# Optimization experiments

Hardware: AMD Instinct MI355X
Metric: run time of the kernel (lower is better)

## Reference

```python
import jax, jax.numpy as jnp
import numpy as np

K_VALUES = (2, 4, 8)  # sorted k_values from init


def setup_inputs() -> dict:
    key = jax.random.key(0)
    ks = jax.random.split(key, 6)
    B, T, D, H = 16, 2048, 512, 64
    nk = len(K_VALUES)
    # columns: (E, Pt, eta, phi) -- E,Pt positive, eta in [-3,3], phi in [-pi,pi]
    u = jax.random.uniform(ks[0], (B, T, 4), jnp.float32)
    tokens_cont = u * jnp.array([100.0, 50.0, 6.0, 6.2832], jnp.float32) + jnp.array([1.0, 1.0, -3.0, -3.1416], jnp.float32)
    lengths = jax.random.randint(ks[1], (B,), T // 2, T + 1)
    mask = jnp.arange(T)[None, :] < lengths[:, None]  # [B,T] True=valid
    W1 = jax.random.normal(ks[2], (nk, H), jnp.float32) / np.sqrt(nk).astype(np.float32)
    b1 = jax.random.normal(ks[3], (H,), jnp.float32) * 0.01
    W2 = jax.random.normal(ks[4], (H, D), jnp.float32) / np.sqrt(H).astype(np.float32)
    b2 = jax.random.normal(ks[5], (D,), jnp.float32) * 0.01
    return dict(tokens_cont=tokens_cont, mask=mask, W1=W1, b1=b1, W2=W2, b2=b2)


def reference(tokens_cont, mask, W1, b1, W2, b2):
    B, T, _ = tokens_cont.shape
    E, Pt, eta, phi = (tokens_cont[..., i] for i in range(4))
    px = Pt * jnp.cos(phi)
    py = Pt * jnp.sin(phi)
    pz = Pt * jnp.sinh(jnp.clip(eta, -20.0, 20.0))
    P = jnp.stack([E, px, py, pz], axis=-1)  # [B,T,4] four-momentum
    metric = jnp.array([1.0, -1.0, -1.0, -1.0], P.dtype)
    # Lorentz dot: E_i E_j - px_i px_j - py_i py_j - pz_i pz_j -> [B,T,T]
    dot = jnp.einsum('btc,bsc->bts', P * metric, P)
    dot = jnp.where(mask[:, None, :], dot, -jnp.inf)  # exclude padding friends
    max_k = min(max(K_VALUES), T)
    _, topk_idx = jax.lax.top_k(dot, max_k)  # [B,T,max_k]
    Pf = P[jnp.arange(B)[:, None, None], topk_idx]  # gather friends [B,T,max_k,4]
    cum = jnp.cumsum(Pf, axis=2)  # prefix sums over sorted friends
    masses = []
    maskf = mask.astype(P.dtype)
    for k in K_VALUES:
        ps = cum[:, :, min(k, max_k) - 1, :]  # [B,T,4] summed 4-momentum of top-k group
        m2 = ps[..., 0] ** 2 - jnp.sum(ps[..., 1:] ** 2, axis=-1)
        m2 = jnp.maximum(m2, 0.0) * maskf
        masses.append(jnp.sqrt(m2 + 1e-8))
    mass = jnp.stack(masses, axis=-1)  # [B,T,n_k]
    h = jax.nn.gelu(mass @ W1 + b1, approximate=False)  # torch GELU = exact erf
    return h @ W2 + b2  # [B,T,model_dim]
```

## Files before the change

kernel.cpp:

```cpp
#include <hip/hip_runtime.h>
#include <hip/hip_bf16.h>
#include <math.h>

#define NB 16
#define NT 2048
#define ND 512
#define NH 64

typedef __attribute__((ext_vector_type(8))) short short8;
typedef __attribute__((ext_vector_type(4))) float float4v;

__device__ __forceinline__ bool mask_is_bytes(const int* m) {
    return m[0] == 0x01010101;
}
__device__ __forceinline__ bool mask_at(const int* m, bool bytes, int i) {
    if (bytes) return ((const unsigned char*)m)[i] != 0;
    return m[i] != 0;
}

__device__ __forceinline__ float dot4(float4 a, float4 p) {
    float d = a.x * p.x;
    d = __builtin_fmaf(a.y, p.y, d);
    d = __builtin_fmaf(a.z, p.z, d);
    d = __builtin_fmaf(a.w, p.w, d);
    return d;
}

__device__ __forceinline__ unsigned short f2bf(float x) {
    unsigned int u = __float_as_uint(x);
    u += 0x7fffu + ((u >> 16) & 1u);
    return (unsigned short)(u >> 16);
}

__global__ void __launch_bounds__(256) prep_kernel(
        const float* __restrict__ tok, const int* __restrict__ mask,
        const float* __restrict__ W2, unsigned short* __restrict__ W2t,
        float4* __restrict__ Pg) {
    int i = blockIdx.x * 256 + threadIdx.x;
    if (i < ND * NH) {
        int n = i & (ND - 1), k = i >> 9;
        W2t[n * NH + k] = f2bf(W2[k * ND + n]);
    } else {
        int j = i - ND * NH;
        const bool mb = mask_is_bytes(mask);
        float4 tv = ((const float4*)tok)[j];
        bool m = mask_at(mask, mb, j);
        float E = tv.x, Pt = tv.y, eta = tv.z, phi = tv.w;
        float px = Pt * cosf(phi);
        float py = Pt * sinf(phi);
        float pz = Pt * sinhf(fminf(fmaxf(eta, -20.f), 20.f));
        Pg[j] = m ? make_float4(E, px, py, pz)
                  : make_float4(-1e30f, 0.f, 0.f, 0.f);
    }
}

#define VT(w2, j, l)  scratch[((w2) * 8 + (j)) * 64 + (l)]
#define PS(w2, c, l)  scratch[((w2) * 12 + (c)) * 64 + (l)]

__global__ void __launch_bounds__(512) fused_topk_mass_mlp_kernel(
        const int* __restrict__ mask,
        const float* __restrict__ W1,
        const float* __restrict__ b1,
        const unsigned short* __restrict__ W2t,
        const float* __restrict__ b2,
        const float4* __restrict__ Pg,
        float* __restrict__ out) {
    __shared__ float scratch[8 * 12 * 64];
    __shared__ unsigned short hs[64][88];
    __shared__ float mass_s[3][64];
    __shared__ int wcnt[8];

    const int b    = blockIdx.y;
    const int t0   = blockIdx.x * 64;
    const int tid  = threadIdx.x;
    const int lane = tid & 63;
    const int w    = tid >> 6;
    const bool mb  = mask_is_bytes(mask);

    const bool blockValid = mask_at(mask, mb, b * NT + t0);

    if (blockValid) {
        int cnt = 0;
#pragma unroll
        for (int it = 0; it < 4; ++it) {
            int i = tid + it * 512;
            bool m = mask_at(mask, mb, b * NT + i);
            cnt += (int)__popcll(__ballot(m));
        }
        if (lane == 0) wcnt[w] = cnt;
        __syncthreads();

        int L = 0;
#pragma unroll
        for (int j = 0; j < 8; ++j) L += wcnt[j];
        const int C    = (L + 7) >> 3;
        const int sBeg = w * C;
        const int sEnd = min(sBeg + C, L);

        const float4* Pb = Pg + (size_t)b * NT;
        float4 pt = Pb[t0 + lane];
        float4 a  = make_float4(pt.x, -pt.y, -pt.z, -pt.w);

        const float NEGBIG = -3.402823466e38f;
        float v0 = NEGBIG, v1 = NEGBIG, v2 = NEGBIG, v3 = NEGBIG;
        float v4 = NEGBIG, v5 = NEGBIG, v6 = NEGBIG, v7 = NEGBIG;

#pragma unroll 8
        for (int s = sBeg; s < sEnd; ++s) {
            float4 ps = Pb[__builtin_amdgcn_readfirstlane(s)];
            float d = dot4(a, ps);
            float n0 = fmaxf(v0, d);
            float n1 = __builtin_amdgcn_fmed3f(d, v0, v1);
            float n2 = __builtin_amdgcn_fmed3f(d, v1, v2);
            float n3 = __builtin_amdgcn_fmed3f(d, v2, v3);
            float n4 = __builtin_amdgcn_fmed3f(d, v3, v4);
            float n5 = __builtin_amdgcn_fmed3f(d, v4, v5);
            float n6 = __builtin_amdgcn_fmed3f(d, v5, v6);
            float n7 = __builtin_amdgcn_fmed3f(d, v6, v7);
            v0 = n0; v1 = n1; v2 = n2; v3 = n3;
            v4 = n4; v5 = n5; v6 = n6; v7 = n7;
        }
        VT(w, 0, lane) = v0; VT(w, 1, lane) = v1;
        VT(w, 2, lane) = v2; VT(w, 3, lane) = v3;
        VT(w, 4, lane) = v4; VT(w, 5, lane) = v5;
        VT(w, 6, lane) = v6; VT(w, 7, lane) = v7;
        __syncthreads();

        float m0 = NEGBIG, m1 = NEGBIG, m2_ = NEGBIG, m3 = NEGBIG;
        float m4 = NEGBIG, m5 = NEGBIG, m6 = NEGBIG, m7 = NEGBIG;
#pragma unroll
        for (int w2 = 0; w2 < 8; ++w2) {
#pragma unroll
            for (int j = 0; j < 8; ++j) {
                float d = VT(w2, j, lane);
                float n0 = fmaxf(m0, d);
                float n1 = __builtin_amdgcn_fmed3f(d, m0, m1);
                float n2 = __builtin_amdgcn_fmed3f(d, m1, m2_);
                float n3 = __builtin_amdgcn_fmed3f(d, m2_, m3);
                float n4 = __builtin_amdgcn_fmed3f(d, m3, m4);
                float n5 = __builtin_amdgcn_fmed3f(d, m4, m5);
                float n6 = __builtin_amdgcn_fmed3f(d, m5, m6);
                float n7 = __builtin_amdgcn_fmed3f(d, m6, m7);
                m0 = n0; m1 = n1; m2_ = n2; m3 = n3;
                m4 = n4; m5 = n5; m6 = n6; m7 = n7;
            }
        }
        const float th2 = m1, th4 = m3, th8 = m7;
        __syncthreads();

        float s2x = 0.f, s2y = 0.f, s2z = 0.f, s2w = 0.f;
        float s4x = 0.f, s4y = 0.f, s4z = 0.f, s4w = 0.f;
        float s8x = 0.f, s8y = 0.f, s8z = 0.f, s8w = 0.f;
#pragma unroll 4
        for (int s = sBeg; s < sEnd; ++s) {
            float4 ps = Pb[__builtin_amdgcn_readfirstlane(s)];
            float d = dot4(a, ps);
            if (d >= th8) {
                s8x += ps.x; s8y += ps.y; s8z += ps.z; s8w += ps.w;
                if (d >= th4) {
                    s4x += ps.x; s4y += ps.y; s4z += ps.z; s4w += ps.w;
                    if (d >= th2) {
                        s2x += ps.x; s2y += ps.y; s2z += ps.z; s2w += ps.w;
                    }
                }
            }
        }
        PS(w, 0, lane) = s2x;  PS(w, 1, lane) = s2y;
        PS(w, 2, lane) = s2z;  PS(w, 3, lane) = s2w;
        PS(w, 4, lane) = s4x;  PS(w, 5, lane) = s4y;
        PS(w, 6, lane) = s4z;  PS(w, 7, lane) = s4w;
        PS(w, 8, lane) = s8x;  PS(w, 9, lane) = s8y;
        PS(w, 10, lane) = s8z; PS(w, 11, lane) = s8w;
        __syncthreads();

        if (w == 0) {
            float tot[12];
#pragma unroll
            for (int c = 0; c < 12; ++c) {
                float acc = 0.f;
#pragma unroll
                for (int w2 = 0; w2 < 8; ++w2) acc += PS(w2, c, lane);
                tot[c] = acc;
            }
            const bool maskt = (t0 + lane) < L;
            const float MZ = sqrtf(1e-8f);
            auto massf = [&](float sx, float sy, float sz, float sw) -> float {
                float q = sx * sx;
                q = __builtin_fmaf(-sy, sy, q);
                q = __builtin_fmaf(-sz, sz, q);
                q = __builtin_fmaf(-sw, sw, q);
                q = fmaxf(q, 0.f);
                return sqrtf(q + 1e-8f);
            };
            mass_s[0][lane] = maskt ? massf(tot[0], tot[1], tot[2], tot[3]) : MZ;
            mass_s[1][lane] = maskt ? massf(tot[4], tot[5], tot[6], tot[7]) : MZ;
            mass_s[2][lane] = maskt ? massf(tot[8], tot[9], tot[10], tot[11]) : MZ;
        }
    } else {
        if (tid < 64) {
            const float MZ = sqrtf(1e-8f);
            mass_s[0][tid] = MZ;
            mass_s[1][tid] = MZ;
            mass_s[2][tid] = MZ;
        }
    }
    __syncthreads();

    {
        const int tt = lane;
        const int hr = w;
        float q0 = mass_s[0][tt];
        float q1 = mass_s[1][tt];
        float q2 = mass_s[2][tt];
        unsigned short hv[8];
#pragma unroll
        for (int j = 0; j < 8; ++j) {
            int hh = hr * 8 + j;
            float pre = b1[hh];
            pre = __builtin_fmaf(q0, W1[hh], pre);
            pre = __builtin_fmaf(q1, W1[NH + hh], pre);
            pre = __builtin_fmaf(q2, W1[2 * NH + hh], pre);
            float g = 0.5f * pre * (1.0f + erff(pre * 0.70710678118654752f));
            hv[j] = f2bf(g);
        }
        *(short8*)&hs[tt][hr * 8] = *(const short8*)hv;
    }
    __syncthreads();

    const int col   = lane & 15;
    const int quad  = lane >> 4;
    const int mhalf = w >> 2;
    const int nBase = (w & 3) * 128;

    short8 afrag[2][2];
#pragma unroll
    for (int mt = 0; mt < 2; ++mt)
#pragma unroll
        for (int ks = 0; ks < 2; ++ks)
            afrag[mt][ks] = *(const short8*)&hs[mhalf * 32 + mt * 16 + col][ks * 32 + quad * 8];

    float4v acc[2][8];
#pragma unroll
    for (int mt = 0; mt < 2; ++mt)
#pragma unroll
        for (int nt = 0; nt < 8; ++nt)
            acc[mt][nt] = (float4v)(0.f);

#pragma unroll
    for (int nt = 0; nt < 8; ++nt) {
        const unsigned short* wp = W2t + (nBase + nt * 16 + col) * NH + quad * 8;
        short8 bf0 = *(const short8*)(wp);
        short8 bf1 = *(const short8*)(wp + 32);
        acc[0][nt] = __builtin_amdgcn_mfma_f32_16x16x32_bf16(afrag[0][0], bf0, acc[0][nt], 0, 0, 0);
        acc[1][nt] = __builtin_amdgcn_mfma_f32_16x16x32_bf16(afrag[1][0], bf0, acc[1][nt], 0, 0, 0);
        acc[0][nt] = __builtin_amdgcn_mfma_f32_16x16x32_bf16(afrag[0][1], bf1, acc[0][nt], 0, 0, 0);
        acc[1][nt] = __builtin_amdgcn_mfma_f32_16x16x32_bf16(afrag[1][1], bf1, acc[1][nt], 0, 0, 0);
    }

#pragma unroll
    for (int nt = 0; nt < 8; ++nt) {
        float bias = b2[nBase + nt * 16 + col];
#pragma unroll
        for (int mt = 0; mt < 2; ++mt) {
            int mRow = b * NT + t0 + mhalf * 32 + mt * 16 + quad * 4;
            size_t base = (size_t)mRow * ND + nBase + nt * 16 + col;
#pragma unroll
            for (int r = 0; r < 4; ++r) {
                out[base + (size_t)r * ND] = acc[mt][nt][r] + bias;
            }
        }
    }
}

extern "C" void kernel_launch(void* const* d_in, const int* in_sizes, int n_in,
                              void* d_out, int out_size, void* d_ws, size_t ws_size,
                              hipStream_t stream) {
    const float* tok  = (const float*)d_in[0];
    const int*   mask = (const int*)d_in[1];
    const float* W1   = (const float*)d_in[2];
    const float* b1   = (const float*)d_in[3];
    const float* W2   = (const float*)d_in[4];
    const float* b2   = (const float*)d_in[5];
    float*       out  = (float*)d_out;

    unsigned short* W2t = (unsigned short*)d_ws;
    float4*         Pg  = (float4*)((char*)d_ws + 0x10000);

    prep_kernel<<<dim3((ND * NH + NB * NT) / 256), dim3(256), 0, stream>>>(
        tok, mask, W2, W2t, Pg);

    dim3 gB(NT / 64, NB);
    fused_topk_mass_mlp_kernel<<<gB, dim3(512), 0, stream>>>(
        mask, W1, b1, W2t, b2, Pg, out);
}
```

Baseline: 163.6 us.

## Remap top-k search to one query per wave with register-cached candidates

Each wave now handles 8 queries one at a time. All 2048 candidate four-momenta are cached in registers, 32 per lane, and spread across the 64 lanes. The per-lane top-8 is merged by eight rounds of DPP wave-max pops, and the group sums are reduced with DPP wave sums, so the shared-memory scratch and the block-wide syncs for merging go away. The cost is much more serialized cross-lane work per query and heavy register pressure from the 32 float4 values per lane, which could hurt occupancy despite the launch_bounds(512,2) hint.

```diff
diff --git a/kernel.cpp b/kernel.cpp
--- a/kernel.cpp
+++ b/kernel.cpp
@@ -18,18 +18,37 @@
     return m[i] != 0;
 }
 
-__device__ __forceinline__ float dot4(float4 a, float4 p) {
-    float d = a.x * p.x;
-    d = __builtin_fmaf(a.y, p.y, d);
-    d = __builtin_fmaf(a.z, p.z, d);
-    d = __builtin_fmaf(a.w, p.w, d);
-    return d;
-}
-
 __device__ __forceinline__ unsigned short f2bf(float x) {
     unsigned int u = __float_as_uint(x);
     u += 0x7fffu + ((u >> 16) & 1u);
     return (unsigned short)(u >> 16);
+}
+
+__device__ __forceinline__ float rlane(float x, int j) {
+    return __int_as_float(__builtin_amdgcn_readlane(__float_as_int(x), j));
+}
+
+template <int CTRL>
+__device__ __forceinline__ float updpp(float x, int identBits) {
+    return __int_as_float(__builtin_amdgcn_update_dpp(
+        identBits, __float_as_int(x), CTRL, 0xF, 0xF, false));
+}
+__device__ __forceinline__ float wave_max(float m) {
+    const int NI = (int)0xFF800000u;
+    m = fmaxf(m, updpp<0x111>(m, NI));
+    m = fmaxf(m, updpp<0x112>(m, NI));
+    m = fmaxf(m, updpp<0x114>(m, NI));
+    m = fmaxf(m, updpp<0x118>(m, NI));
+    float a = rlane(m, 15), bb = rlane(m, 31);
+    float c = rlane(m, 47), d  = rlane(m, 63);
+    return fmaxf(fmaxf(a, bb), fmaxf(c, d));
+}
+__device__ __forceinline__ float wave_sum(float x) {
+    x += updpp<0x111>(x, 0);
+    x += updpp<0x112>(x, 0);
+    x += updpp<0x114>(x, 0);
+    x += updpp<0x118>(x, 0);
+    return (rlane(x, 15) + rlane(x, 31)) + (rlane(x, 47) + rlane(x, 63));
 }
 
 __global__ void __launch_bounds__(256) prep_kernel(
@@ -54,10 +73,7 @@
     }
 }
 
-#define VT(w2, j, l)  scratch[((w2) * 8 + (j)) * 64 + (l)]
-#define PS(w2, c, l)  scratch[((w2) * 12 + (c)) * 64 + (l)]
-
-__global__ void __launch_bounds__(512) fused_topk_mass_mlp_kernel(
+__global__ void __launch_bounds__(512, 2) fused_topk_mass_mlp_kernel(
         const int* __restrict__ mask,
         const float* __restrict__ W1,
         const float* __restrict__ b1,
@@ -65,7 +81,6 @@
         const float* __restrict__ b2,
         const float4* __restrict__ Pg,
         float* __restrict__ out) {
-    __shared__ float scratch[8 * 12 * 64];
     __shared__ unsigned short hs[64][88];
     __shared__ float mass_s[3][64];
     __shared__ int wcnt[8];
@@ -76,6 +91,8 @@
     const int lane = tid & 63;
     const int w    = tid >> 6;
     const bool mb  = mask_is_bytes(mask);
+    const float NEGBIG = -3.402823466e38f;
+    const float MZ = sqrtf(1e-8f);
 
     const bool blockValid = mask_at(mask, mb, b * NT + t0);
 
@@ -84,121 +101,128 @@
 #pragma unroll
         for (int it = 0; it < 4; ++it) {
             int i = tid + it * 512;
-            bool m = mask_at(mask, mb, b * NT + i);
-            cnt += (int)__popcll(__ballot(m));
+            cnt += (int)__popcll(__ballot(mask_at(mask, mb, b * NT + i)));
         }
         if (lane == 0) wcnt[w] = cnt;
         __syncthreads();
-
         int L = 0;
 #pragma unroll
         for (int j = 0; j < 8; ++j) L += wcnt[j];
-        const int C    = (L + 7) >> 3;
-        const int sBeg = w * C;
-        const int sEnd = min(sBeg + C, L);
-
-        const float4* Pb = Pg + (size_t)b * NT;
+        const int RACT = (L + 63) >> 6;
+
+        const float4* __restrict__ Pb = Pg + (size_t)b * NT;
         float4 pt = Pb[t0 + lane];
-        float4 a  = make_float4(pt.x, -pt.y, -pt.z, -pt.w);
-
-        const float NEGBIG = -3.402823466e38f;
-        float v0 = NEGBIG, v1 = NEGBIG, v2 = NEGBIG, v3 = NEGBIG;
-        float v4 = NEGBIG, v5 = NEGBIG, v6 = NEGBIG, v7 = NEGBIG;
-
-#pragma unroll 8
-        for (int s = sBeg; s < sEnd; ++s) {
-            float4 ps = Pb[__builtin_amdgcn_readfirstlane(s)];
-            float d = dot4(a, ps);
-            float n0 = fmaxf(v0, d);
-            float n1 = __builtin_amdgcn_fmed3f(d, v0, v1);
-            float n2 = __builtin_amdgcn_fmed3f(d, v1, v2);
-            float n3 = __builtin_amdgcn_fmed3f(d, v2, v3);
-            float n4 = __builtin_amdgcn_fmed3f(d, v3, v4);
-            float n5 = __builtin_amdgcn_fmed3f(d, v4, v5);
-            float n6 = __builtin_amdgcn_fmed3f(d, v5, v6);
-            float n7 = __builtin_amdgcn_fmed3f(d, v6, v7);
-            v0 = n0; v1 = n1; v2 = n2; v3 = n3;
-            v4 = n4; v5 = n5; v6 = n6; v7 = n7;
-        }
-        VT(w, 0, lane) = v0; VT(w, 1, lane) = v1;
-        VT(w, 2, lane) = v2; VT(w, 3, lane) = v3;
-        VT(w, 4, lane) = v4; VT(w, 5, lane) = v5;
-        VT(w, 6, lane) = v6; VT(w, 7, lane) = v7;
-        __syncthreads();
-
-        float m0 = NEGBIG, m1 = NEGBIG, m2_ = NEGBIG, m3 = NEGBIG;
-        float m4 = NEGBIG, m5 = NEGBIG, m6 = NEGBIG, m7 = NEGBIG;
-#pragma unroll
-        for (int w2 = 0; w2 < 8; ++w2) {
-#pragma unroll
-            for (int j = 0; j < 8; ++j) {
-                float d = VT(w2, j, lane);
-                float n0 = fmaxf(m0, d);
-                float n1 = __builtin_amdgcn_fmed3f(d, m0, m1);
-                float n2 = __builtin_amdgcn_fmed3f(d, m1, m2_);
-                float n3 = __builtin_amdgcn_fmed3f(d, m2_, m3);
-                float n4 = __builtin_amdgcn_fmed3f(d, m3, m4);
-                float n5 = __builtin_amdgcn_fmed3f(d, m4, m5);
-                float n6 = __builtin_amdgcn_fmed3f(d, m5, m6);
-                float n7 = __builtin_amdgcn_fmed3f(d, m6, m7);
-                m0 = n0; m1 = n1; m2_ = n2; m3 = n3;
-                m4 = n4; m5 = n5; m6 = n6; m7 = n7;
+
+        float4 cr[32];
+#pragma unroll
+        for (int r = 0; r < 32; ++r) cr[r] = Pb[r * 64 + lane];
+
+#pragma unroll 1
+        for (int q = 0; q < 8; ++q) {
+            const int ql = w * 8 + q;
+            if (t0 + ql < L) {
+                const float Eq  =  rlane(pt.x, ql);
+                const float npx = -rlane(pt.y, ql);
+                const float npy = -rlane(pt.z, ql);
+                const float npz = -rlane(pt.w, ql);
+
+                float v0 = NEGBIG, v1 = NEGBIG, v2 = NEGBIG, v3 = NEGBIG;
+                float v4 = NEGBIG, v5 = NEGBIG, v6 = NEGBIG, v7 = NEGBIG;
+#pragma unroll
+                for (int r = 0; r < 32; ++r) {
+                    if (r < RACT) {
+                        float d = Eq * cr[r].x;
+                        d = __builtin_fmaf(npx, cr[r].y, d);
+                        d = __builtin_fmaf(npy, cr[r].z, d);
+                        d = __builtin_fmaf(npz, cr[r].w, d);
+                        float n0 = fmaxf(v0, d);
+                        float n1 = __builtin_amdgcn_fmed3f(d, v0, v1);
+                        float n2 = __builtin_amdgcn_fmed3f(d, v1, v2);
+                        float n3 = __builtin_amdgcn_fmed3f(d, v2, v3);
+                        float n4 = __builtin_amdgcn_fmed3f(d, v3, v4);
+                        float n5 = __builtin_amdgcn_fmed3f(d, v4, v5);
+                        float n6 = __builtin_amdgcn_fmed3f(d, v5, v6);
+                        float n7 = __builtin_amdgcn_fmed3f(d, v6, v7);
+                        v0 = n0; v1 = n1; v2 = n2; v3 = n3;
+                        v4 = n4; v5 = n5; v6 = n6; v7 = n7;
+                    }
+                }
+
+                float th2 = NEGBIG, th4 = NEGBIG, th8 = NEGBIG;
+#pragma unroll
+                for (int round = 1; round <= 8; ++round) {
+                    float gm = wave_max(v0);
+                    if (round == 2) th2 = gm;
+                    if (round == 4) th4 = gm;
+                    if (round == 8) th8 = gm;
+                    if (round < 8) {
+                        bool pop = (v0 == gm);
+                        v0 = pop ? v1 : v0;
+                        v1 = pop ? v2 : v1;
+                        v2 = pop ? v3 : v2;
+                        v3 = pop ? v4 : v3;
+                        v4 = pop ? v5 : v4;
+                        v5 = pop ? v6 : v5;
+                        v6 = pop ? v7 : v6;
+                        v7 = pop ? NEGBIG : v7;
+                    }
+                }
+
+                float s2x = 0.f, s2y = 0.f, s2z = 0.f, s2w = 0.f;
+                float s4x = 0.f, s4y = 0.f, s4z = 0.f, s4w = 0.f;
+                float s8x = 0.f, s8y = 0.f, s8z = 0.f, s8w = 0.f;
+#pragma unroll
+                for (int r = 0; r < 32; ++r) {
+                    if (r < RACT) {
+                        float d = Eq * cr[r].x;
+                        d = __builtin_fmaf(npx, cr[r].y, d);
+                        d = __builtin_fmaf(npy, cr[r].z, d);
+                        d = __builtin_fmaf(npz, cr[r].w, d);
+                        if (d >= th8) {
+                            s8x += cr[r].x; s8y += cr[r].y;
+                            s8z += cr[r].z; s8w += cr[r].w;
+                            if (d >= th4) {
+                                s4x += cr[r].x; s4y += cr[r].y;
+                                s4z += cr[r].z; s4w += cr[r].w;
+                                if (d >= th2) {
+                                    s2x += cr[r].x; s2y += cr[r].y;
+                                    s2z += cr[r].z; s2w += cr[r].w;
+                                }
+                            }
+                        }
+                    }
+                }
+
+                float t2x = wave_sum(s2x), t2y = wave_sum(s2y);
+                float t2z = wave_sum(s2z), t2w = wave_sum(s2w);
+                float t4x = wave_sum(s4x), t4y = wave_sum(s4y);
+                float t4z = wave_sum(s4z), t4w = wave_sum(s4w);
+                float t8x = wave_sum(s8x), t8y = wave_sum(s8y);
+                float t8z = wave_sum(s8z), t8w = wave_sum(s8w);
+
+                auto massf = [&](float sx, float sy, float sz, float sw) -> float {
+                    float qq = sx * sx;
+                    qq = __builtin_fmaf(-sy, sy, qq);
+                    qq = __builtin_fmaf(-sz, sz, qq);
+                    qq = __builtin_fmaf(-sw, sw, qq);
+                    qq = fmaxf(qq, 0.f);
+                    return sqrtf(qq + 1e-8f);
+                };
+                if (lane == 0) {
+                    mass_s[0][ql] = massf(t2x, t2y, t2z, t2w);
+                    mass_s[1][ql] = massf(t4x, t4y, t4z, t4w);
+                    mass_s[2][ql] = massf(t8x, t8y, t8z, t8w);
+                }
+            } else {
+                if (lane == 0) {
+                    mass_s[0][ql] = MZ;
+                    mass_s[1][ql] = MZ;
+                    mass_s[2][ql] = MZ;
+                }
             }
-        }
-        const float th2 = m1, th4 = m3, th8 = m7;
-        __syncthreads();
-
-        float s2x = 0.f, s2y = 0.f, s2z = 0.f, s2w = 0.f;
-        float s4x = 0.f, s4y = 0.f, s4z = 0.f, s4w = 0.f;
-        float s8x = 0.f, s8y = 0.f, s8z = 0.f, s8w = 0.f;
-#pragma unroll 4
-        for (int s = sBeg; s < sEnd; ++s) {
-            float4 ps = Pb[__builtin_amdgcn_readfirstlane(s)];
-            float d = dot4(a, ps);
-            if (d >= th8) {
-                s8x += ps.x; s8y += ps.y; s8z += ps.z; s8w += ps.w;
-                if (d >= th4) {
-                    s4x += ps.x; s4y += ps.y; s4z += ps.z; s4w += ps.w;
-                    if (d >= th2) {
-                        s2x += ps.x; s2y += ps.y; s2z += ps.z; s2w += ps.w;
-                    }
-                }
-            }
-        }
-        PS(w, 0, lane) = s2x;  PS(w, 1, lane) = s2y;
-        PS(w, 2, lane) = s2z;  PS(w, 3, lane) = s2w;
-        PS(w, 4, lane) = s4x;  PS(w, 5, lane) = s4y;
-        PS(w, 6, lane) = s4z;  PS(w, 7, lane) = s4w;
-        PS(w, 8, lane) = s8x;  PS(w, 9, lane) = s8y;
-        PS(w, 10, lane) = s8z; PS(w, 11, lane) = s8w;
-        __syncthreads();
-
-        if (w == 0) {
-            float tot[12];
-#pragma unroll
-            for (int c = 0; c < 12; ++c) {
-                float acc = 0.f;
-#pragma unroll
-                for (int w2 = 0; w2 < 8; ++w2) acc += PS(w2, c, lane);
-                tot[c] = acc;
-            }
-            const bool maskt = (t0 + lane) < L;
-            const float MZ = sqrtf(1e-8f);
-            auto massf = [&](float sx, float sy, float sz, float sw) -> float {
-                float q = sx * sx;
-                q = __builtin_fmaf(-sy, sy, q);
-                q = __builtin_fmaf(-sz, sz, q);
-                q = __builtin_fmaf(-sw, sw, q);
-                q = fmaxf(q, 0.f);
-                return sqrtf(q + 1e-8f);
-            };
-            mass_s[0][lane] = maskt ? massf(tot[0], tot[1], tot[2], tot[3]) : MZ;
-            mass_s[1][lane] = maskt ? massf(tot[4], tot[5], tot[6], tot[7]) : MZ;
-            mass_s[2][lane] = maskt ? massf(tot[8], tot[9], tot[10], tot[11]) : MZ;
         }
     } else {
         if (tid < 64) {
-            const float MZ = sqrtf(1e-8f);
             mass_s[0][tid] = MZ;
             mass_s[1][tid] = MZ;
             mass_s[2][tid] = MZ;
```

Measured after the change: 184.9 us. 13.0% more time.

## Pair query tiles per block and stage batch four-momenta in LDS

Applied to the files above, without the earlier changes.

Each block now handles two 64-token query tiles, one from the first half and one from the second half of the sequence. Pairing them balances work across blocks, since every block gets an always-valid tile A plus a tile B that may be padding. The whole batch's four-momenta are copied into LDS once, and each candidate load is shared between both query tiles in the top-k and accumulation passes. The cost is a much larger LDS footprint (about 80KB), which lowers occupancy, plus more registers for the doubled chains and a serialized two-pass MLP epilogue.

```diff
diff --git a/kernel.cpp b/kernel.cpp
--- a/kernel.cpp
+++ b/kernel.cpp
@@ -31,6 +31,19 @@
     u += 0x7fffu + ((u >> 16) & 1u);
     return (unsigned short)(u >> 16);
 }
+
+#define CHAIN8(v0,v1,v2,v3,v4,v5,v6,v7,d) do {                 \
+    float n0 = fmaxf(v0, d);                                    \
+    float n1 = __builtin_amdgcn_fmed3f(d, v0, v1);              \
+    float n2 = __builtin_amdgcn_fmed3f(d, v1, v2);              \
+    float n3 = __builtin_amdgcn_fmed3f(d, v2, v3);              \
+    float n4 = __builtin_amdgcn_fmed3f(d, v3, v4);              \
+    float n5 = __builtin_amdgcn_fmed3f(d, v4, v5);              \
+    float n6 = __builtin_amdgcn_fmed3f(d, v5, v6);              \
+    float n7 = __builtin_amdgcn_fmed3f(d, v6, v7);              \
+    v0 = n0; v1 = n1; v2 = n2; v3 = n3;                         \
+    v4 = n4; v5 = n5; v6 = n6; v7 = n7;                         \
+} while (0)
 
 __global__ void __launch_bounds__(256) prep_kernel(
         const float* __restrict__ tok, const int* __restrict__ mask,
@@ -54,8 +67,10 @@
     }
 }
 
-#define VT(w2, j, l)  scratch[((w2) * 8 + (j)) * 64 + (l)]
-#define PS(w2, c, l)  scratch[((w2) * 12 + (c)) * 64 + (l)]
+#define VTA(w2, j, l)  scratch[((w2) * 8 + (j)) * 64 + (l)]
+#define VTB(w2, j, l)  scratch[4096 + ((w2) * 8 + (j)) * 64 + (l)]
+#define PSA(w2, c, l)  scratch[((w2) * 12 + (c)) * 64 + (l)]
+#define PSB(w2, c, l)  scratch[6144 + ((w2) * 12 + (c)) * 64 + (l)]
 
 __global__ void __launch_bounds__(512) fused_topk_mass_mlp_kernel(
         const int* __restrict__ mask,
@@ -65,165 +80,216 @@
         const float* __restrict__ b2,
         const float4* __restrict__ Pg,
         float* __restrict__ out) {
-    __shared__ float scratch[8 * 12 * 64];
-    __shared__ unsigned short hs[64][88];
-    __shared__ float mass_s[3][64];
+    __shared__ __align__(16) unsigned char smem_raw[32768 + 49152];
     __shared__ int wcnt[8];
+    float* Plds            = (float*)smem_raw;
+    float* scratch         = (float*)(smem_raw + 32768);
+    unsigned short (*hs)[88] = (unsigned short(*)[88])smem_raw;
+    float (*mass_s)[128]   = (float(*)[128])(smem_raw + 12288);
 
     const int b    = blockIdx.y;
-    const int t0   = blockIdx.x * 64;
+    const int x    = blockIdx.x;
+    const int tA   = 64 * x;
+    const int tB   = 1024 + 64 * x;
     const int tid  = threadIdx.x;
     const int lane = tid & 63;
     const int w    = tid >> 6;
     const bool mb  = mask_is_bytes(mask);
-
-    const bool blockValid = mask_at(mask, mb, b * NT + t0);
-
-    if (blockValid) {
-        int cnt = 0;
-#pragma unroll
-        for (int it = 0; it < 4; ++it) {
-            int i = tid + it * 512;
-            bool m = mask_at(mask, mb, b * NT + i);
-            cnt += (int)__popcll(__ballot(m));
-        }
-        if (lane == 0) wcnt[w] = cnt;
-        __syncthreads();
-
-        int L = 0;
-#pragma unroll
-        for (int j = 0; j < 8; ++j) L += wcnt[j];
-        const int C    = (L + 7) >> 3;
-        const int sBeg = w * C;
-        const int sEnd = min(sBeg + C, L);
-
-        const float4* Pb = Pg + (size_t)b * NT;
-        float4 pt = Pb[t0 + lane];
-        float4 a  = make_float4(pt.x, -pt.y, -pt.z, -pt.w);
-
-        const float NEGBIG = -3.402823466e38f;
-        float v0 = NEGBIG, v1 = NEGBIG, v2 = NEGBIG, v3 = NEGBIG;
-        float v4 = NEGBIG, v5 = NEGBIG, v6 = NEGBIG, v7 = NEGBIG;
-
-#pragma unroll 8
+    const float NEGBIG = -3.402823466e38f;
+    const float MZ = sqrtf(1e-8f);
+
+    int cnt = 0;
+    const float4* __restrict__ Pb = Pg + (size_t)b * NT;
+#pragma unroll
+    for (int it = 0; it < 4; ++it) {
+        int i = tid + it * 512;
+        *(float4*)&Plds[i * 4] = Pb[i];
+        cnt += (int)__popcll(__ballot(mask_at(mask, mb, b * NT + i)));
+    }
+    if (lane == 0) wcnt[w] = cnt;
+    __syncthreads();
+
+    int L = 0;
+#pragma unroll
+    for (int j = 0; j < 8; ++j) L += wcnt[j];
+    const int C    = (L + 7) >> 3;
+    const int sBeg = w * C;
+    const int sEnd = min(sBeg + C, L);
+    const bool hasB = tB < L;
+
+    float4 pA = *(const float4*)&Plds[(tA + lane) * 4];
+    float4 pBq = *(const float4*)&Plds[(tB + lane) * 4];
+    float4 aA = make_float4(pA.x, -pA.y, -pA.z, -pA.w);
+    float4 aB = make_float4(pBq.x, -pBq.y, -pBq.z, -pBq.w);
+
+    float vA0 = NEGBIG, vA1 = NEGBIG, vA2 = NEGBIG, vA3 = NEGBIG;
+    float vA4 = NEGBIG, vA5 = NEGBIG, vA6 = NEGBIG, vA7 = NEGBIG;
+    float vB0 = NEGBIG, vB1 = NEGBIG, vB2 = NEGBIG, vB3 = NEGBIG;
+    float vB4 = NEGBIG, vB5 = NEGBIG, vB6 = NEGBIG, vB7 = NEGBIG;
+
+    if (hasB) {
+#pragma unroll 4
         for (int s = sBeg; s < sEnd; ++s) {
-            float4 ps = Pb[__builtin_amdgcn_readfirstlane(s)];
-            float d = dot4(a, ps);
-            float n0 = fmaxf(v0, d);
-            float n1 = __builtin_amdgcn_fmed3f(d, v0, v1);
-            float n2 = __builtin_amdgcn_fmed3f(d, v1, v2);
-            float n3 = __builtin_amdgcn_fmed3f(d, v2, v3);
-            float n4 = __builtin_amdgcn_fmed3f(d, v3, v4);
-            float n5 = __builtin_amdgcn_fmed3f(d, v4, v5);
-            float n6 = __builtin_amdgcn_fmed3f(d, v5, v6);
-            float n7 = __builtin_amdgcn_fmed3f(d, v6, v7);
-            v0 = n0; v1 = n1; v2 = n2; v3 = n3;
-            v4 = n4; v5 = n5; v6 = n6; v7 = n7;
-        }
-        VT(w, 0, lane) = v0; VT(w, 1, lane) = v1;
-        VT(w, 2, lane) = v2; VT(w, 3, lane) = v3;
-        VT(w, 4, lane) = v4; VT(w, 5, lane) = v5;
-        VT(w, 6, lane) = v6; VT(w, 7, lane) = v7;
-        __syncthreads();
-
+            float4 ps = *(const float4*)&Plds[s * 4];
+            float dA = dot4(aA, ps);
+            float dB = dot4(aB, ps);
+            CHAIN8(vA0, vA1, vA2, vA3, vA4, vA5, vA6, vA7, dA);
+            CHAIN8(vB0, vB1, vB2, vB3, vB4, vB5, vB6, vB7, dB);
+        }
+    } else {
+#pragma unroll 4
+        for (int s = sBeg; s < sEnd; ++s) {
+            float4 ps = *(const float4*)&Plds[s * 4];
+            float dA = dot4(aA, ps);
+            CHAIN8(vA0, vA1, vA2, vA3, vA4, vA5, vA6, vA7, dA);
+        }
+    }
+    VTA(w, 0, lane) = vA0; VTA(w, 1, lane) = vA1;
+    VTA(w, 2, lane) = vA2; VTA(w, 3, lane) = vA3;
+    VTA(w, 4, lane) = vA4; VTA(w, 5, lane) = vA5;
+    VTA(w, 6, lane) = vA6; VTA(w, 7, lane) = vA7;
+    if (hasB) {
+        VTB(w, 0, lane) = vB0; VTB(w, 1, lane) = vB1;
+        VTB(w, 2, lane) = vB2; VTB(w, 3, lane) = vB3;
+        VTB(w, 4, lane) = vB4; VTB(w, 5, lane) = vB5;
+        VTB(w, 6, lane) = vB6; VTB(w, 7, lane) = vB7;
+    }
+    __syncthreads();
+
+    float thA2, thA4, thA8;
+    {
         float m0 = NEGBIG, m1 = NEGBIG, m2_ = NEGBIG, m3 = NEGBIG;
         float m4 = NEGBIG, m5 = NEGBIG, m6 = NEGBIG, m7 = NEGBIG;
 #pragma unroll
-        for (int w2 = 0; w2 < 8; ++w2) {
+        for (int w2 = 0; w2 < 8; ++w2)
 #pragma unroll
             for (int j = 0; j < 8; ++j) {
-                float d = VT(w2, j, lane);
-                float n0 = fmaxf(m0, d);
-                float n1 = __builtin_amdgcn_fmed3f(d, m0, m1);
-                float n2 = __builtin_amdgcn_fmed3f(d, m1, m2_);
-                float n3 = __builtin_amdgcn_fmed3f(d, m2_, m3);
-                float n4 = __builtin_amdgcn_fmed3f(d, m3, m4);
-                float n5 = __builtin_amdgcn_fmed3f(d, m4, m5);
-                float n6 = __builtin_amdgcn_fmed3f(d, m5, m6);
-                float n7 = __builtin_amdgcn_fmed3f(d, m6, m7);
-                m0 = n0; m1 = n1; m2_ = n2; m3 = n3;
-                m4 = n4; m5 = n5; m6 = n6; m7 = n7;
-            }
-        }
-        const float th2 = m1, th4 = m3, th8 = m7;
-        __syncthreads();
-
-        float s2x = 0.f, s2y = 0.f, s2z = 0.f, s2w = 0.f;
-        float s4x = 0.f, s4y = 0.f, s4z = 0.f, s4w = 0.f;
-        float s8x = 0.f, s8y = 0.f, s8z = 0.f, s8w = 0.f;
+                float d = VTA(w2, j, lane);
+                CHAIN8(m0, m1, m2_, m3, m4, m5, m6, m7, d);
+            }
+        thA2 = m1; thA4 = m3; thA8 = m7;
+    }
+    float thB2 = 0.f, thB4 = 0.f, thB8 = 0.f;
+    if (hasB) {
+        float m0 = NEGBIG, m1 = NEGBIG, m2_ = NEGBIG, m3 = NEGBIG;
+        float m4 = NEGBIG, m5 = NEGBIG, m6 = NEGBIG, m7 = NEGBIG;
+#pragma unroll
+        for (int w2 = 0; w2 < 8; ++w2)
+#pragma unroll
+            for (int j = 0; j < 8; ++j) {
+                float d = VTB(w2, j, lane);
+                CHAIN8(m0, m1, m2_, m3, m4, m5, m6, m7, d);
+            }
+        thB2 = m1; thB4 = m3; thB8 = m7;
+    }
+    __syncthreads();
+
+    {
+        float a2x = 0.f, a2y = 0.f, a2z = 0.f, a2w = 0.f;
+        float a4x = 0.f, a4y = 0.f, a4z = 0.f, a4w = 0.f;
+        float a8x = 0.f, a8y = 0.f, a8z = 0.f, a8w = 0.f;
+        float b2x = 0.f, b2y = 0.f, b2z = 0.f, b2w = 0.f;
+        float b4x = 0.f, b4y = 0.f, b4z = 0.f, b4w = 0.f;
+        float b8x = 0.f, b8y = 0.f, b8z = 0.f, b8w = 0.f;
+        if (hasB) {
 #pragma unroll 4
-        for (int s = sBeg; s < sEnd; ++s) {
-            float4 ps = Pb[__builtin_amdgcn_readfirstlane(s)];
-            float d = dot4(a, ps);
-            if (d >= th8) {
-                s8x += ps.x; s8y += ps.y; s8z += ps.z; s8w += ps.w;
-                if (d >= th4) {
-                    s4x += ps.x; s4y += ps.y; s4z += ps.z; s4w += ps.w;
-                    if (d >= th2) {
-                        s2x += ps.x; s2y += ps.y; s2z += ps.z; s2w += ps.w;
+            for (int s = sBeg; s < sEnd; ++s) {
+                float4 ps = *(const float4*)&Plds[s * 4];
+                float dA = dot4(aA, ps);
+                float dB = dot4(aB, ps);
+                if (dA >= thA8) {
+                    a8x += ps.x; a8y += ps.y; a8z += ps.z; a8w += ps.w;
+                    if (dA >= thA4) {
+                        a4x += ps.x; a4y += ps.y; a4z += ps.z; a4w += ps.w;
+                        if (dA >= thA2) {
+                            a2x += ps.x; a2y += ps.y; a2z += ps.z; a2w += ps.w;
+                        }
                     }
                 }
-            }
-        }
-        PS(w, 0, lane) = s2x;  PS(w, 1, lane) = s2y;
-        PS(w, 2, lane) = s2z;  PS(w, 3, lane) = s2w;
-        PS(w, 4, lane) = s4x;  PS(w, 5, lane) = s4y;
-        PS(w, 6, lane) = s4z;  PS(w, 7, lane) = s4w;
-        PS(w, 8, lane) = s8x;  PS(w, 9, lane) = s8y;
-        PS(w, 10, lane) = s8z; PS(w, 11, lane) = s8w;
-        __syncthreads();
-
+                if (dB >= thB8) {
+                    b8x += ps.x; b8y += ps.y; b8z += ps.z; b8w += ps.w;
+                    if (dB >= thB4) {
+                        b4x += ps.x; b4y += ps.y; b4z += ps.z; b4w += ps.w;
+                        if (dB >= thB2) {
+                            b2x += ps.x; b2y += ps.y; b2z += ps.z; b2w += ps.w;
+                        }
+                    }
+                }
+            }
+        } else {
+#pragma unroll 4
+            for (int s = sBeg; s < sEnd; ++s) {
+                float4 ps = *(const float4*)&Plds[s * 4];
+                float dA = dot4(aA, ps);
+                if (dA >= thA8) {
+                    a8x += ps.x; a8y += ps.y; a8z += ps.z; a8w += ps.w;
+                    if (dA >= thA4) {
+                        a4x += ps.x; a4y += ps.y; a4z += ps.z; a4w += ps.w;
+                        if (dA >= thA2) {
+                            a2x += ps.x; a2y += ps.y; a2z += ps.z; a2w += ps.w;
+                        }
+                    }
+                }
+            }
+        }
+        PSA(w, 0, lane) = a2x;  PSA(w, 1, lane) = a2y;
+        PSA(w, 2, lane) = a2z;  PSA(w, 3, lane) = a2w;
+        PSA(w, 4, lane) = a4x;  PSA(w, 5, lane) = a4y;
+        PSA(w, 6, lane) = a4z;  PSA(w, 7, lane) = a4w;
+        PSA(w, 8, lane) = a8x;  PSA(w, 9, lane) = a8y;
+        PSA(w, 10, lane) = a8z; PSA(w, 11, lane) = a8w;
+        if (hasB) {
+            PSB(w, 0, lane) = b2x;  PSB(w, 1, lane) = b2y;
+            PSB(w, 2, lane) = b2z;  PSB(w, 3, lane) = b2w;
+            PSB(w, 4, lane) = b4x;  PSB(w, 5, lane) = b4y;
+            PSB(w, 6, lane) = b4z;  PSB(w, 7, lane) = b4w;
+            PSB(w, 8, lane) = b8x;  PSB(w, 9, lane) = b8y;
+            PSB(w, 10, lane) = b8z; PSB(w, 11, lane) = b8w;
+        }
+    }
+    __syncthreads();
+
+    {
+        auto massf = [](float sx, float sy, float sz, float sw) -> float {
+            float q = sx * sx;
+            q = __builtin_fmaf(-sy, sy, q);
+            q = __builtin_fmaf(-sz, sz, q);
+            q = __builtin_fmaf(-sw, sw, q);
+            q = fmaxf(q, 0.f);
+            return sqrtf(q + 1e-8f);
+        };
         if (w == 0) {
             float tot[12];
 #pragma unroll
             for (int c = 0; c < 12; ++c) {
                 float acc = 0.f;
 #pragma unroll
-                for (int w2 = 0; w2 < 8; ++w2) acc += PS(w2, c, lane);
+                for (int w2 = 0; w2 < 8; ++w2) acc += PSA(w2, c, lane);
                 tot[c] = acc;
             }
-            const bool maskt = (t0 + lane) < L;
-            const float MZ = sqrtf(1e-8f);
-            auto massf = [&](float sx, float sy, float sz, float sw) -> float {
-                float q = sx * sx;
-                q = __builtin_fmaf(-sy, sy, q);
-                q = __builtin_fmaf(-sz, sz, q);
-                q = __builtin_fmaf(-sw, sw, q);
-                q = fmaxf(q, 0.f);
-                return sqrtf(q + 1e-8f);
-            };
-            mass_s[0][lane] = maskt ? massf(tot[0], tot[1], tot[2], tot[3]) : MZ;
-            mass_s[1][lane] = maskt ? massf(tot[4], tot[5], tot[6], tot[7]) : MZ;
-            mass_s[2][lane] = maskt ? massf(tot[8], tot[9], tot[10], tot[11]) : MZ;
-        }
-    } else {
-        if (tid < 64) {
-            const float MZ = sqrtf(1e-8f);
-            mass_s[0][tid] = MZ;
-            mass_s[1][tid] = MZ;
-            mass_s[2][tid] = MZ;
-        }
-    }
-    __syncthreads();
-
-    {
-        const int tt = lane;
-        const int hr = w;
-        float q0 = mass_s[0][tt];
-        float q1 = mass_s[1][tt];
-        float q2 = mass_s[2][tt];
-        unsigned short hv[8];
-#pragma unroll
-        for (int j = 0; j < 8; ++j) {
-            int hh = hr * 8 + j;
-            float pre = b1[hh];
-            pre = __builtin_fmaf(q0, W1[hh], pre);
-            pre = __builtin_fmaf(q1, W1[NH + hh], pre);
-            pre = __builtin_fmaf(q2, W1[2 * NH + hh], pre);
-            float g = 0.5f * pre * (1.0f + erff(pre * 0.70710678118654752f));
-            hv[j] = f2bf(g);
-        }
-        *(short8*)&hs[tt][hr * 8] = *(const short8*)hv;
+            mass_s[0][lane] = massf(tot[0], tot[1], tot[2], tot[3]);
+            mass_s[1][lane] = massf(tot[4], tot[5], tot[6], tot[7]);
+            mass_s[2][lane] = massf(tot[8], tot[9], tot[10], tot[11]);
+        } else if (w == 1) {
+            if (hasB) {
+                float tot[12];
+#pragma unroll
+                for (int c = 0; c < 12; ++c) {
+                    float acc = 0.f;
+#pragma unroll
+                    for (int w2 = 0; w2 < 8; ++w2) acc += PSB(w2, c, lane);
+                    tot[c] = acc;
+                }
+                const bool maskt = (tB + lane) < L;
+                mass_s[0][64 + lane] = maskt ? massf(tot[0], tot[1], tot[2], tot[3]) : MZ;
+                mass_s[1][64 + lane] = maskt ? massf(tot[4], tot[5], tot[6], tot[7]) : MZ;
+                mass_s[2][64 + lane] = maskt ? massf(tot[8], tot[9], tot[10], tot[11]) : MZ;
+            } else {
+                mass_s[0][64 + lane] = MZ;
+                mass_s[1][64 + lane] = MZ;
+                mass_s[2][64 + lane] = MZ;
+            }
+        }
     }
     __syncthreads();
 
@@ -232,41 +298,66 @@
     const int mhalf = w >> 2;
     const int nBase = (w & 3) * 128;
 
-    short8 afrag[2][2];
-#pragma unroll
-    for (int mt = 0; mt < 2; ++mt)
-#pragma unroll
-        for (int ks = 0; ks < 2; ++ks)
-            afrag[mt][ks] = *(const short8*)&hs[mhalf * 32 + mt * 16 + col][ks * 32 + quad * 8];
-
-    float4v acc[2][8];
-#pragma unroll
-    for (int mt = 0; mt < 2; ++mt)
-#pragma unroll
-        for (int nt = 0; nt < 8; ++nt)
-            acc[mt][nt] = (float4v)(0.f);
-
-#pragma unroll
-    for (int nt = 0; nt < 8; ++nt) {
-        const unsigned short* wp = W2t + (nBase + nt * 16 + col) * NH + quad * 8;
-        short8 bf0 = *(const short8*)(wp);
-        short8 bf1 = *(const short8*)(wp + 32);
-        acc[0][nt] = __builtin_amdgcn_mfma_f32_16x16x32_bf16(afrag[0][0], bf0, acc[0][nt], 0, 0, 0);
-        acc[1][nt] = __builtin_amdgcn_mfma_f32_16x16x32_bf16(afrag[1][0], bf0, acc[1][nt], 0, 0, 0);
-        acc[0][nt] = __builtin_amdgcn_mfma_f32_16x16x32_bf16(afrag[0][1], bf1, acc[0][nt], 0, 0, 0);
-        acc[1][nt] = __builtin_amdgcn_mfma_f32_16x16x32_bf16(afrag[1][1], bf1, acc[1][nt], 0, 0, 0);
-    }
-
-#pragma unroll
-    for (int nt = 0; nt < 8; ++nt) {
-        float bias = b2[nBase + nt * 16 + col];
-#pragma unroll
-        for (int mt = 0; mt < 2; ++mt) {
-            int mRow = b * NT + t0 + mhalf * 32 + mt * 16 + quad * 4;
-            size_t base = (size_t)mRow * ND + nBase + nt * 16 + col;
-#pragma unroll
-            for (int r = 0; r < 4; ++r) {
-                out[base + (size_t)r * ND] = acc[mt][nt][r] + bias;
+#pragma unroll 1
+    for (int m = 0; m < 2; ++m) {
+        if (m) __syncthreads();
+
+        {
+            float q0 = mass_s[0][m * 64 + lane];
+            float q1 = mass_s[1][m * 64 + lane];
+            float q2 = mass_s[2][m * 64 + lane];
+            unsigned short hv[8];
+#pragma unroll
+            for (int j = 0; j < 8; ++j) {
+                int hh = w * 8 + j;
+                float pre = b1[hh];
+                pre = __builtin_fmaf(q0, W1[hh], pre);
+                pre = __builtin_fmaf(q1, W1[NH + hh], pre);
+                pre = __builtin_fmaf(q2, W1[2 * NH + hh], pre);
+                float g = 0.5f * pre * (1.0f + erff(pre * 0.70710678118654752f));
+                hv[j] = f2bf(g);
+            }
+            *(short8*)&hs[lane][w * 8] = *(const short8*)hv;
+        }
+        __syncthreads();
+
+        short8 afrag[2][2];
+#pragma unroll
+        for (int mt = 0; mt < 2; ++mt)
+#pragma unroll
+            for (int ks = 0; ks < 2; ++ks)
+                afrag[mt][ks] = *(const short8*)&hs[mhalf * 32 + mt * 16 + col][ks * 32 + quad * 8];
+
+        float4v acc[2][8];
+#pragma unroll
+        for (int mt = 0; mt < 2; ++mt)
+#pragma unroll
+            for (int nt = 0; nt < 8; ++nt)
+                acc[mt][nt] = (float4v)(0.f);
+
+#pragma unroll
+        for (int nt = 0; nt < 8; ++nt) {
+            const unsigned short* wp = W2t + (nBase + nt * 16 + col) * NH + quad * 8;
+            short8 bf0 = *(const short8*)(wp);
+            short8 bf1 = *(const short8*)(wp + 32);
+            acc[0][nt] = __builtin_amdgcn_mfma_f32_16x16x32_bf16(afrag[0][0], bf0, acc[0][nt], 0, 0, 0);
+            acc[1][nt] = __builtin_amdgcn_mfma_f32_16x16x32_bf16(afrag[1][0], bf0, acc[1][nt], 0, 0, 0);
+            acc[0][nt] = __builtin_amdgcn_mfma_f32_16x16x32_bf16(afrag[0][1], bf1, acc[0][nt], 0, 0, 0);
+            acc[1][nt] = __builtin_amdgcn_mfma_f32_16x16x32_bf16(afrag[1][1], bf1, acc[1][nt], 0, 0, 0);
+        }
+
+        const int tileBase = b * NT + (m ? tB : tA);
+#pragma unroll
+        for (int nt = 0; nt < 8; ++nt) {
+            float bias = b2[nBase + nt * 16 + col];
+#pragma unroll
+            for (int mt = 0; mt < 2; ++mt) {
+                int mRow = tileBase + mhalf * 32 + mt * 16 + quad * 4;
+                size_t base = (size_t)mRow * ND + nBase + nt * 16 + col;
+#pragma unroll
+                for (int r = 0; r < 4; ++r) {
+                    out[base + (size_t)r * ND] = acc[mt][nt][r] + bias;
+                }
             }
         }
     }
@@ -289,7 +380,7 @@
     prep_kernel<<<dim3((ND * NH + NB * NT) / 256), dim3(256), 0, stream>>>(
         tok, mask, W2, W2t, Pg);
 
-    dim3 gB(NT / 64, NB);
+    dim3 gB(NT / 128, NB);
     fused_topk_mass_mlp_kernel<<<gB, dim3(512), 0, stream>>>(
         mask, W1, b1, W2t, b2, Pg, out);
 }
```

Measured after the change: 144.7 us. -11.5%, faster.
